# Kernel tuning notes

Measured on AMD Instinct MI355X. Metric: run time of the kernel, lower is better.

The kernel has to match this reference:

```python
import jax, jax.numpy as jnp
import numpy as np

N_USER, N_SPOT, D = 100000, 50000, 128
E_VISIT, E_REV, E_NEAR = 500000, 500000, 200000
P_DROP = 0.1


def _glorot(k, fan_in, fan_out):
    lim = jnp.sqrt(6.0 / (fan_in + fan_out))
    return jax.random.uniform(k, (fan_in, fan_out), jnp.float32, -lim, lim)


def setup_inputs() -> dict:
    key = jax.random.key(0)
    ks = jax.random.split(key, 14)
    return {
        "x_user": jax.random.normal(ks[0], (N_USER, D), jnp.float32),
        "x_spot": jax.random.normal(ks[1], (N_SPOT, D), jnp.float32),
        "W_visit_src": _glorot(ks[2], D, D),   # user side of (user,visit,spot)
        "W_visit_tgt": _glorot(ks[3], D, D),   # spot side of (user,visit,spot)
        "W_rev_src": _glorot(ks[4], D, D),     # spot side of (spot,visited_by,user)
        "W_rev_tgt": _glorot(ks[5], D, D),     # user side of (spot,visited_by,user)
        "W_near_src": _glorot(ks[6], D, D),    # (spot,near,spot)
        "W_near_tgt": _glorot(ks[7], D, D),
        "visit_src": jax.random.randint(ks[8], (E_VISIT,), 0, N_USER, jnp.int64),
        "visit_dst": jax.random.randint(ks[9], (E_VISIT,), 0, N_SPOT, jnp.int64),
        "rev_src": jax.random.randint(ks[10], (E_REV,), 0, N_SPOT, jnp.int64),
        "rev_dst": jax.random.randint(ks[11], (E_REV,), 0, N_USER, jnp.int64),
        "near_src": jax.random.randint(ks[12], (E_NEAR,), 0, N_SPOT, jnp.int64),
        "near_dst": jax.random.randint(ks[13], (E_NEAR,), 0, N_SPOT, jnp.int64),
    }


def _scatter_mean(vals, idx, n_seg):
    # scatter(..., reduce='mean') into zeros: empty segments stay 0
    s = jax.ops.segment_sum(vals, idx, num_segments=n_seg)
    c = jax.ops.segment_sum(jnp.ones((vals.shape[0],), vals.dtype), idx, num_segments=n_seg)
    return s / jnp.maximum(c, 1.0)[:, None]


def _edge_type(x_src, x_tgt, W_src, W_tgt, src_idx, dst_idx, n_tgt, dkey):
    src_p = x_src @ W_src                      # [N_src, D]
    tgt_p = x_tgt @ W_tgt                      # [N_tgt, D]
    g = src_p[src_idx]                         # gather per edge [E, D]
    keep = jax.random.bernoulli(dkey, 1.0 - P_DROP, g.shape)
    g = jnp.where(keep, g / (1.0 - P_DROP), jnp.zeros_like(g))  # dropout (training)
    return tgt_p + _scatter_mean(g, dst_idx, n_tgt)


def reference(x_user, x_spot, W_visit_src, W_visit_tgt, W_rev_src, W_rev_tgt,
              W_near_src, W_near_tgt, visit_src, visit_dst, rev_src, rev_dst,
              near_src, near_dst):
    dk = jax.random.key(1)
    spot_a = _edge_type(x_user, x_spot, W_visit_src, W_visit_tgt,
                        visit_src, visit_dst, N_SPOT, jax.random.fold_in(dk, 0))
    user_a = _edge_type(x_spot, x_user, W_rev_src, W_rev_tgt,
                        rev_src, rev_dst, N_USER, jax.random.fold_in(dk, 1))
    spot_b = _edge_type(x_spot, x_spot, W_near_src, W_near_tgt,
                        near_src, near_dst, N_SPOT, jax.random.fold_in(dk, 2))
    # div: spot receives from 2 edge types, user from 1
    out_user = jax.nn.relu(user_a / 1.0)
    out_spot = jax.nn.relu((spot_a + spot_b) / 2.0)
    # ReLU=True applies a second relu (no-op after the first, kept for faithfulness)
    return jax.nn.relu(out_user), jax.nn.relu(out_spot)
```

## Files before the change

kernel.cpp:

```cpp
#include <hip/hip_runtime.h>
#include <stdint.h>

#define DF 128
typedef unsigned short ushort_t;
typedef __attribute__((ext_vector_type(8))) short short8v;
typedef __attribute__((ext_vector_type(4))) float f32x4;

__host__ __device__ __forceinline__ unsigned rotl32(unsigned v, int r) {
  return __builtin_rotateleft32(v, (unsigned)r);
}

__host__ __device__ __forceinline__ void threefry2x32(
    unsigned k0, unsigned k1, unsigned c0, unsigned c1,
    unsigned& o0, unsigned& o1) {
  unsigned kx = k0 ^ k1 ^ 0x1BD11BDAu;
  unsigned x0 = c0 + k0;
  unsigned x1 = c1 + k1;
#define TF_R(r) { x0 += x1; x1 = rotl32(x1, r); x1 ^= x0; }
  TF_R(13) TF_R(15) TF_R(26) TF_R(6)
  x0 += k1; x1 += kx + 1u;
  TF_R(17) TF_R(29) TF_R(16) TF_R(24)
  x0 += kx; x1 += k0 + 2u;
  TF_R(13) TF_R(15) TF_R(26) TF_R(6)
  x0 += k0; x1 += k1 + 3u;
  TF_R(17) TF_R(29) TF_R(16) TF_R(24)
  x0 += k1; x1 += kx + 4u;
  TF_R(13) TF_R(15) TF_R(26) TF_R(6)
  x0 += kx; x1 += k0 + 5u;
#undef TF_R
  o0 = x0; o1 = x1;
}

#define KEEP_THR 0xE6666600u

__device__ __forceinline__ ushort_t f2bf(float f) {
  unsigned u = __float_as_uint(f);
  unsigned r = (u + 0x7fffu + ((u >> 16) & 1u)) >> 16;
  return (ushort_t)r;
}
__device__ __forceinline__ float bf2f(ushort_t h) {
  return __uint_as_float(((unsigned)h) << 16);
}
__device__ __forceinline__ unsigned umin_u(unsigned a, unsigned b) {
  return a < b ? a : b;
}

template <int EPI>
__global__ __launch_bounds__(256) void gemm_mfma(
    const float* __restrict__ X, const float* __restrict__ W1,
    const float* __restrict__ W2, int M,
    ushort_t* __restrict__ outB, float* __restrict__ outF,
    const ushort_t* __restrict__ m1, const ushort_t* __restrict__ m2) {
  __shared__ ushort_t Wt[DF][136];
  const int t = threadIdx.x;
  const int lane = t & 63;
  const int w = t >> 6;
  const int lr = lane & 15;
  const int kg = lane >> 4;
  const int rbase = blockIdx.x * 128;

#pragma unroll
  for (int i = 0; i < 16; ++i) {
    int q = t + i * 256;
    int k = q >> 5;
    int c4 = (q & 31) * 4;
    float4 wv = *reinterpret_cast<const float4*>(&W1[k * DF + c4]);
    if constexpr (EPI == 2) {
      float4 w2 = *reinterpret_cast<const float4*>(&W2[k * DF + c4]);
      wv.x += w2.x; wv.y += w2.y; wv.z += w2.z; wv.w += w2.w;
    }
    Wt[c4 + 0][k] = f2bf(wv.x);
    Wt[c4 + 1][k] = f2bf(wv.y);
    Wt[c4 + 2][k] = f2bf(wv.z);
    Wt[c4 + 3][k] = f2bf(wv.w);
  }
  __syncthreads();

  f32x4 acc[2][8];
#pragma unroll
  for (int rg = 0; rg < 2; ++rg)
#pragma unroll
    for (int n = 0; n < 8; ++n) acc[rg][n] = (f32x4){0.f, 0.f, 0.f, 0.f};

#pragma unroll
  for (int kt = 0; kt < 4; ++kt) {
    const int kb = kt * 32 + kg * 8;
    short8v a[2];
#pragma unroll
    for (int rg = 0; rg < 2; ++rg) {
      int r = rbase + w * 32 + rg * 16 + lr;
      float4 x0 = make_float4(0.f, 0.f, 0.f, 0.f);
      float4 x1 = x0;
      if (r < M) {
        x0 = *reinterpret_cast<const float4*>(&X[(size_t)r * DF + kb]);
        x1 = *reinterpret_cast<const float4*>(&X[(size_t)r * DF + kb + 4]);
      }
      short8v av;
      av[0] = (short)f2bf(x0.x); av[1] = (short)f2bf(x0.y);
      av[2] = (short)f2bf(x0.z); av[3] = (short)f2bf(x0.w);
      av[4] = (short)f2bf(x1.x); av[5] = (short)f2bf(x1.y);
      av[6] = (short)f2bf(x1.z); av[7] = (short)f2bf(x1.w);
      a[rg] = av;
    }
#pragma unroll
    for (int n = 0; n < 8; ++n) {
      short8v b = *reinterpret_cast<const short8v*>(&Wt[n * 16 + lr][kb]);
#pragma unroll
      for (int rg = 0; rg < 2; ++rg)
        acc[rg][n] = __builtin_amdgcn_mfma_f32_16x16x32_bf16(a[rg], b, acc[rg][n], 0, 0, 0);
    }
  }

#pragma unroll
  for (int rg = 0; rg < 2; ++rg) {
    const int rb = rbase + w * 32 + rg * 16 + kg * 4;
#pragma unroll
    for (int n = 0; n < 8; ++n) {
      const int col = n * 16 + lr;
#pragma unroll
      for (int j = 0; j < 4; ++j) {
        const int r = rb + j;
        if (r < M) {
          float vv = acc[rg][n][j];
          if (EPI == 0) {
            outB[(size_t)r * DF + col] = f2bf(vv);
          } else if (EPI == 1) {
            outF[(size_t)r * DF + col] =
                fmaxf(vv + bf2f(m1[(size_t)r * DF + col]), 0.f);
          } else {
            outF[(size_t)r * DF + col] =
                fmaxf(0.5f * (vv + bf2f(m1[(size_t)r * DF + col])
                                 + bf2f(m2[(size_t)r * DF + col])), 0.f);
          }
        }
      }
    }
  }
}

__global__ __launch_bounds__(256) void hist3(
    const int* __restrict__ vd, const int* __restrict__ rd,
    const int* __restrict__ nd, unsigned* __restrict__ deg_all,
    int Ev, int Er, int En, int segU, int segN) {
  int i = blockIdx.x * 256 + threadIdx.x;
  if (i < Ev) atomicAdd(&deg_all[vd[i]], 1u);
  else if (i < Ev + Er) atomicAdd(&deg_all[segU + rd[i - Ev]], 1u);
  else if (i < Ev + Er + En) atomicAdd(&deg_all[segN + nd[i - Ev - Er]], 1u);
}

#define SCAN_E 2048

__global__ __launch_bounds__(256) void scanA(
    const unsigned* __restrict__ deg, unsigned* __restrict__ bsum, int NT) {
  __shared__ unsigned sm[256];
  const int t = threadIdx.x;
  const int base = blockIdx.x * SCAN_E + t * 8;
  unsigned s = 0;
#pragma unroll
  for (int j = 0; j < 8; ++j) {
    int i = base + j;
    s += (i < NT) ? deg[i] : 0u;
  }
  sm[t] = s;
  __syncthreads();
  for (int off = 128; off; off >>= 1) {
    if (t < off) sm[t] += sm[t + off];
    __syncthreads();
  }
  if (t == 0) bsum[blockIdx.x] = sm[0];
}

__global__ __launch_bounds__(1024) void scanB(
    unsigned* __restrict__ bsum, unsigned* __restrict__ rp_all,
    int nb, int NT) {
  __shared__ unsigned sm[1024];
  const int t = threadIdx.x;
  unsigned v = (t < nb) ? bsum[t] : 0u;
  sm[t] = v;
  __syncthreads();
  for (int off = 1; off < 1024; off <<= 1) {
    unsigned u = (t >= off) ? sm[t - off] : 0u;
    __syncthreads();
    sm[t] += u;
    __syncthreads();
  }
  if (t < nb) bsum[t] = sm[t] - v;
  if (t == nb - 1) rp_all[NT] = sm[t];
}

__global__ __launch_bounds__(256) void scanC(
    const unsigned* __restrict__ deg, const unsigned* __restrict__ bsum,
    unsigned* __restrict__ rp, unsigned* __restrict__ cur, int NT) {
  __shared__ unsigned sm[256];
  const int t = threadIdx.x;
  const int base = blockIdx.x * SCAN_E + t * 8;
  unsigned vals[8];
  unsigned s = 0;
#pragma unroll
  for (int j = 0; j < 8; ++j) {
    int i = base + j;
    vals[j] = (i < NT) ? deg[i] : 0u;
    s += vals[j];
  }
  sm[t] = s;
  __syncthreads();
  for (int off = 1; off < 256; off <<= 1) {
    unsigned u = (t >= off) ? sm[t - off] : 0u;
    __syncthreads();
    sm[t] += u;
    __syncthreads();
  }
  unsigned run = bsum[blockIdx.x] + sm[t] - s;
#pragma unroll
  for (int j = 0; j < 8; ++j) {
    int i = base + j;
    if (i < NT) { rp[i] = run; cur[i] = run; }
    run += vals[j];
  }
}

__global__ __launch_bounds__(256) void fill3(
    const int* __restrict__ vs, const int* __restrict__ vd,
    const int* __restrict__ rs, const int* __restrict__ rd,
    const int* __restrict__ ns, const int* __restrict__ nd,
    unsigned* __restrict__ cur_all, uint2* __restrict__ es_all,
    int Ev, int Er, int En, int segU, int segN) {
  int i = blockIdx.x * 256 + threadIdx.x;
  if (i < Ev) {
    unsigned slot = atomicAdd(&cur_all[vd[i]], 1u);
    es_all[slot] = make_uint2((unsigned)i, (unsigned)vs[i]);
  } else if (i < Ev + Er) {
    int e = i - Ev;
    unsigned slot = atomicAdd(&cur_all[segU + rd[e]], 1u);
    es_all[slot] = make_uint2((unsigned)e, (unsigned)rs[e]);
  } else if (i < Ev + Er + En) {
    int e = i - Ev - Er;
    unsigned slot = atomicAdd(&cur_all[segN + nd[e]], 1u);
    es_all[slot] = make_uint2((unsigned)e, (unsigned)ns[e]);
  }
}

__global__ __launch_bounds__(256) void gather_reduce_all(
    const ushort_t* __restrict__ proj_v, const ushort_t* __restrict__ proj_r,
    const ushort_t* __restrict__ proj_n, const uint2* __restrict__ es,
    const unsigned* __restrict__ rp, ushort_t* __restrict__ accum_all,
    int NT, int segU, int segN, unsigned emax,
    unsigned kv0, unsigned kv1, unsigned kr0, unsigned kr1,
    unsigned kn0, unsigned kn1) {
  const int lane = threadIdx.x & 63;
  int d = blockIdx.x * 4 + (threadIdx.x >> 6);
  d = __builtin_amdgcn_readfirstlane(d);
  if (d >= NT) return;

  const ushort_t* proj;
  unsigned k0, k1;
  if (d < segU)      { proj = proj_v; k0 = kv0; k1 = kv1; }
  else if (d < segN) { proj = proj_r; k0 = kr0; k1 = kr1; }
  else               { proj = proj_n; k0 = kn0; k1 = kn1; }

  const unsigned b0 = __builtin_amdgcn_readfirstlane(rp[d]);
  const unsigned n  = __builtin_amdgcn_readfirstlane(rp[d + 1]) - b0;

  const bool hi = lane >= 32;
  const unsigned l31 = (unsigned)(lane & 31);
  const unsigned voff8 = l31 * 8u;

  const unsigned npairs = n >> 1;
  const unsigned odd = n & 1u;

  uint2 P0 = es[umin_u(b0, emax)];
  uint2 P1 = es[umin_u(b0 + 1u, emax)];
  unsigned eA = __builtin_amdgcn_readfirstlane(P0.x);
  unsigned sA = __builtin_amdgcn_readfirstlane(P0.y);
  unsigned eB = __builtin_amdgcn_readfirstlane(P1.x);
  unsigned sB = __builtin_amdgcn_readfirstlane(P1.y);

  float a0 = 0.f, a1 = 0.f, a2 = 0.f, a3 = 0.f;

  for (unsigned p = 0; p < npairs; ++p) {
    const unsigned src = hi ? sB : sA;
    const unsigned eid = hi ? eB : eA;
    const uint2 g = *reinterpret_cast<const uint2*>(
        reinterpret_cast<const char*>(proj) + ((size_t)src << 8) + voff8);
    uint2 Pn0 = es[umin_u(b0 + 2u * p + 2u, emax)];
    uint2 Pn1 = es[umin_u(b0 + 2u * p + 3u, emax)];

    const unsigned cb = eid * 128u + l31 * 4u;
    unsigned r0a, r0b, r1a, r1b, r2a, r2b, r3a, r3b;
    threefry2x32(k0, k1, 0u, cb + 0u, r0a, r0b);
    threefry2x32(k0, k1, 0u, cb + 1u, r1a, r1b);
    threefry2x32(k0, k1, 0u, cb + 2u, r2a, r2b);
    threefry2x32(k0, k1, 0u, cb + 3u, r3a, r3b);
    const float m0 = ((r0a ^ r0b) < KEEP_THR) ? (1.0f / 0.9f) : 0.f;
    const float m1 = ((r1a ^ r1b) < KEEP_THR) ? (1.0f / 0.9f) : 0.f;
    const float m2 = ((r2a ^ r2b) < KEEP_THR) ? (1.0f / 0.9f) : 0.f;
    const float m3 = ((r3a ^ r3b) < KEEP_THR) ? (1.0f / 0.9f) : 0.f;
    a0 = fmaf(__uint_as_float(g.x << 16), m0, a0);
    a1 = fmaf(__uint_as_float(g.x & 0xffff0000u), m1, a1);
    a2 = fmaf(__uint_as_float(g.y << 16), m2, a2);
    a3 = fmaf(__uint_as_float(g.y & 0xffff0000u), m3, a3);

    eA = __builtin_amdgcn_readfirstlane(Pn0.x);
    sA = __builtin_amdgcn_readfirstlane(Pn0.y);
    eB = __builtin_amdgcn_readfirstlane(Pn1.x);
    sB = __builtin_amdgcn_readfirstlane(Pn1.y);
  }

  if (odd) {
    const uint2 g = *reinterpret_cast<const uint2*>(
        reinterpret_cast<const char*>(proj) + ((size_t)sA << 8) + voff8);
    const unsigned cb = eA * 128u + l31 * 4u;
    unsigned r0a, r0b, r1a, r1b, r2a, r2b, r3a, r3b;
    threefry2x32(k0, k1, 0u, cb + 0u, r0a, r0b);
    threefry2x32(k0, k1, 0u, cb + 1u, r1a, r1b);
    threefry2x32(k0, k1, 0u, cb + 2u, r2a, r2b);
    threefry2x32(k0, k1, 0u, cb + 3u, r3a, r3b);
    const float sc = hi ? 0.f : (1.0f / 0.9f);
    const float m0 = ((r0a ^ r0b) < KEEP_THR) ? sc : 0.f;
    const float m1 = ((r1a ^ r1b) < KEEP_THR) ? sc : 0.f;
    const float m2 = ((r2a ^ r2b) < KEEP_THR) ? sc : 0.f;
    const float m3 = ((r3a ^ r3b) < KEEP_THR) ? sc : 0.f;
    a0 = fmaf(__uint_as_float(g.x << 16), m0, a0);
    a1 = fmaf(__uint_as_float(g.x & 0xffff0000u), m1, a1);
    a2 = fmaf(__uint_as_float(g.y << 16), m2, a2);
    a3 = fmaf(__uint_as_float(g.y & 0xffff0000u), m3, a3);
  }

  a0 += __shfl_xor(a0, 32);
  a1 += __shfl_xor(a1, 32);
  a2 += __shfl_xor(a2, 32);
  a3 += __shfl_xor(a3, 32);

  const float inv = 1.0f / fmaxf((float)n, 1.0f);
  const float u0 = hi ? a2 : a0;
  const float u1 = hi ? a3 : a1;
  const unsigned pk =
      ((unsigned)f2bf(u0 * inv)) | (((unsigned)f2bf(u1 * inv)) << 16);
  unsigned* out = reinterpret_cast<unsigned*>(accum_all) + (size_t)d * 64;
  out[2u * l31 + (hi ? 1u : 0u)] = pk;
}

extern "C" void kernel_launch(void* const* d_in, const int* in_sizes, int n_in,
                              void* d_out, int out_size, void* d_ws, size_t ws_size,
                              hipStream_t stream) {
  const float* x_user      = (const float*)d_in[0];
  const float* x_spot      = (const float*)d_in[1];
  const float* W_visit_src = (const float*)d_in[2];
  const float* W_visit_tgt = (const float*)d_in[3];
  const float* W_rev_src   = (const float*)d_in[4];
  const float* W_rev_tgt   = (const float*)d_in[5];
  const float* W_near_src  = (const float*)d_in[6];
  const float* W_near_tgt  = (const float*)d_in[7];
  const int* visit_src = (const int*)d_in[8];
  const int* visit_dst = (const int*)d_in[9];
  const int* rev_src   = (const int*)d_in[10];
  const int* rev_dst   = (const int*)d_in[11];
  const int* near_src  = (const int*)d_in[12];
  const int* near_dst  = (const int*)d_in[13];

  const int n_user = in_sizes[0] / DF;
  const int n_spot = in_sizes[1] / DF;
  const int e_visit = in_sizes[8];
  const int e_rev   = in_sizes[10];
  const int e_near  = in_sizes[12];

  float* out_user = (float*)d_out;
  float* out_spot = out_user + (size_t)n_user * DF;

  const int NT = n_spot + n_user + n_spot;
  const int segU = n_spot;
  const int segN = n_spot + n_user;
  const int etot = e_visit + e_rev + e_near;
  const unsigned emax = (unsigned)(etot - 1);

  char* ws = (char*)d_ws;
  size_t off = 0;
  auto alloc = [&](size_t bytes) -> void* {
    void* p = ws + off;
    off += (bytes + 255) & ~(size_t)255;
    return p;
  };
  ushort_t* proj_vs   = (ushort_t*)alloc((size_t)n_user * DF * 2);
  ushort_t* proj_rs   = (ushort_t*)alloc((size_t)n_spot * DF * 2);
  ushort_t* proj_ns   = (ushort_t*)alloc((size_t)n_spot * DF * 2);
  ushort_t* accum_all = (ushort_t*)alloc((size_t)NT * DF * 2);
  uint2*    es_all    = (uint2*)   alloc((size_t)etot * 8);
  unsigned* rp_all    = (unsigned*)alloc(((size_t)NT + 1) * 4);
  unsigned* cur_all   = (unsigned*)alloc((size_t)NT * 4);
  unsigned* deg_all   = (unsigned*)alloc((size_t)NT * 4);
  unsigned* bsum      = (unsigned*)alloc(4096);

  ushort_t* mean_sv = accum_all;
  ushort_t* mean_u  = accum_all + (size_t)segU * DF;
  ushort_t* mean_sn = accum_all + (size_t)segN * DF;

  unsigned kv0, kv1, kr0, kr1, kn0, kn1;
  threefry2x32(0u, 1u, 0u, 0u, kv0, kv1);
  threefry2x32(0u, 1u, 0u, 1u, kr0, kr1);
  threefry2x32(0u, 1u, 0u, 2u, kn0, kn1);

  dim3 blk(256);
  const int gb_user = (n_user + 127) / 128;
  const int gb_spot = (n_spot + 127) / 128;
  const int gb_e = (etot + 255) / 256;
  const int nb_scan = (NT + SCAN_E - 1) / SCAN_E;

  hipMemsetAsync(deg_all, 0, (size_t)NT * 4, stream);
  hist3<<<gb_e, blk, 0, stream>>>(visit_dst, rev_dst, near_dst, deg_all,
                                  e_visit, e_rev, e_near, segU, segN);
  scanA<<<nb_scan, blk, 0, stream>>>(deg_all, bsum, NT);
  scanB<<<1, 1024, 0, stream>>>(bsum, rp_all, nb_scan, NT);
  scanC<<<nb_scan, blk, 0, stream>>>(deg_all, bsum, rp_all, cur_all, NT);
  fill3<<<gb_e, blk, 0, stream>>>(visit_src, visit_dst, rev_src, rev_dst,
                                  near_src, near_dst, cur_all, es_all,
                                  e_visit, e_rev, e_near, segU, segN);

  gemm_mfma<0><<<gb_user, blk, 0, stream>>>(x_user, W_visit_src, nullptr, n_user,
                                            proj_vs, nullptr, nullptr, nullptr);
  gemm_mfma<0><<<gb_spot, blk, 0, stream>>>(x_spot, W_rev_src, nullptr, n_spot,
                                            proj_rs, nullptr, nullptr, nullptr);
  gemm_mfma<0><<<gb_spot, blk, 0, stream>>>(x_spot, W_near_src, nullptr, n_spot,
                                            proj_ns, nullptr, nullptr, nullptr);

  gather_reduce_all<<<(NT + 3) / 4, blk, 0, stream>>>(
      proj_vs, proj_rs, proj_ns, es_all, rp_all, accum_all,
      NT, segU, segN, emax, kv0, kv1, kr0, kr1, kn0, kn1);

  gemm_mfma<1><<<gb_user, blk, 0, stream>>>(x_user, W_rev_tgt, nullptr, n_user,
                                            nullptr, out_user, mean_u, nullptr);
  gemm_mfma<2><<<gb_spot, blk, 0, stream>>>(x_spot, W_visit_tgt, W_near_tgt, n_spot,
                                            nullptr, out_spot, mean_sv, mean_sn);
}
```

Baseline: 608.7 us.

## Merge GEMM launches and stage epilogue through LDS for coalesced stores

Combines the three source-projection GEMMs into one launch and the two target GEMMs into another, using block-index dispatch. The epilogue now stages accumulators in shared memory so global writes become 16-byte row-contiguous stores, and mean inputs are read as vectors. This replaces the scattered 2- and 4-byte stores of the MFMA layout and cuts launch overhead, at the cost of a larger shared-memory footprint and extra barriers.

```diff
diff --git a/kernel.cpp b/kernel.cpp
--- a/kernel.cpp
+++ b/kernel.cpp
@@ -38,26 +38,26 @@
   unsigned r = (u + 0x7fffu + ((u >> 16) & 1u)) >> 16;
   return (ushort_t)r;
 }
-__device__ __forceinline__ float bf2f(ushort_t h) {
-  return __uint_as_float(((unsigned)h) << 16);
+__device__ __forceinline__ float bf2f(unsigned h) {
+  return __uint_as_float(h << 16);
 }
 __device__ __forceinline__ unsigned umin_u(unsigned a, unsigned b) {
   return a < b ? a : b;
 }
 
-template <int EPI>
-__global__ __launch_bounds__(256) void gemm_mfma(
+#define WT(k, c) sm_u[(k) * 136 + (c)]
+#define CTB(r, c) sm_u[(r) * 144 + (c)]
+#define CTF(r, c) sm_f[(r) * 68 + (c)]
+
+__device__ __forceinline__ void gemm_core(
     const float* __restrict__ X, const float* __restrict__ W1,
-    const float* __restrict__ W2, int M,
-    ushort_t* __restrict__ outB, float* __restrict__ outF,
-    const ushort_t* __restrict__ m1, const ushort_t* __restrict__ m2) {
-  __shared__ ushort_t Wt[DF][136];
+    const float* __restrict__ W2, bool sumW, int M, int rbase,
+    ushort_t* sm_u, f32x4 acc[2][8]) {
   const int t = threadIdx.x;
   const int lane = t & 63;
   const int w = t >> 6;
   const int lr = lane & 15;
   const int kg = lane >> 4;
-  const int rbase = blockIdx.x * 128;
 
 #pragma unroll
   for (int i = 0; i < 16; ++i) {
@@ -65,18 +65,17 @@
     int k = q >> 5;
     int c4 = (q & 31) * 4;
     float4 wv = *reinterpret_cast<const float4*>(&W1[k * DF + c4]);
-    if constexpr (EPI == 2) {
+    if (sumW) {
       float4 w2 = *reinterpret_cast<const float4*>(&W2[k * DF + c4]);
       wv.x += w2.x; wv.y += w2.y; wv.z += w2.z; wv.w += w2.w;
     }
-    Wt[c4 + 0][k] = f2bf(wv.x);
-    Wt[c4 + 1][k] = f2bf(wv.y);
-    Wt[c4 + 2][k] = f2bf(wv.z);
-    Wt[c4 + 3][k] = f2bf(wv.w);
+    WT(c4 + 0, k) = f2bf(wv.x);
+    WT(c4 + 1, k) = f2bf(wv.y);
+    WT(c4 + 2, k) = f2bf(wv.z);
+    WT(c4 + 3, k) = f2bf(wv.w);
   }
   __syncthreads();
 
-  f32x4 acc[2][8];
 #pragma unroll
   for (int rg = 0; rg < 2; ++rg)
 #pragma unroll
@@ -104,38 +103,135 @@
     }
 #pragma unroll
     for (int n = 0; n < 8; ++n) {
-      short8v b = *reinterpret_cast<const short8v*>(&Wt[n * 16 + lr][kb]);
+      short8v b = *reinterpret_cast<const short8v*>(&WT(n * 16 + lr, kb));
 #pragma unroll
       for (int rg = 0; rg < 2; ++rg)
         acc[rg][n] = __builtin_amdgcn_mfma_f32_16x16x32_bf16(a[rg], b, acc[rg][n], 0, 0, 0);
     }
   }
-
+}
+
+__global__ __launch_bounds__(256) void proj3_gemm(
+    const float* __restrict__ x_user, const float* __restrict__ x_spot,
+    const float* __restrict__ Wv, const float* __restrict__ Wr,
+    const float* __restrict__ Wn, int n_user, int n_spot,
+    ushort_t* __restrict__ pv, ushort_t* __restrict__ pr,
+    ushort_t* __restrict__ pn, int gbU, int gbS) {
+  __shared__ __align__(16) ushort_t sm_u[18432];
+  const int b = blockIdx.x;
+  const float* X; const float* W; ushort_t* out; int M; int rbase;
+  if (b < gbU)            { X = x_user; W = Wv; out = pv; M = n_user; rbase = b * 128; }
+  else if (b < gbU + gbS) { X = x_spot; W = Wr; out = pr; M = n_spot; rbase = (b - gbU) * 128; }
+  else                    { X = x_spot; W = Wn; out = pn; M = n_spot; rbase = (b - gbU - gbS) * 128; }
+
+  f32x4 acc[2][8];
+  gemm_core(X, W, nullptr, false, M, rbase, sm_u, acc);
+
+  const int t = threadIdx.x;
+  const int lane = t & 63;
+  const int w = t >> 6;
+  const int lr = lane & 15;
+  const int kg = lane >> 4;
+
+  __syncthreads();
 #pragma unroll
   for (int rg = 0; rg < 2; ++rg) {
-    const int rb = rbase + w * 32 + rg * 16 + kg * 4;
+    const int rowb = w * 32 + rg * 16 + kg * 4;
 #pragma unroll
     for (int n = 0; n < 8; ++n) {
       const int col = n * 16 + lr;
 #pragma unroll
-      for (int j = 0; j < 4; ++j) {
-        const int r = rb + j;
-        if (r < M) {
-          float vv = acc[rg][n][j];
-          if (EPI == 0) {
-            outB[(size_t)r * DF + col] = f2bf(vv);
-          } else if (EPI == 1) {
-            outF[(size_t)r * DF + col] =
-                fmaxf(vv + bf2f(m1[(size_t)r * DF + col]), 0.f);
-          } else {
-            outF[(size_t)r * DF + col] =
-                fmaxf(0.5f * (vv + bf2f(m1[(size_t)r * DF + col])
-                                 + bf2f(m2[(size_t)r * DF + col])), 0.f);
-          }
-        }
+      for (int j = 0; j < 4; ++j) CTB(rowb + j, col) = f2bf(acc[rg][n][j]);
+    }
+  }
+  __syncthreads();
+#pragma unroll
+  for (int i = 0; i < 8; ++i) {
+    const int u = t + i * 256;
+    const int row = u >> 4, ch = u & 15;
+    const int grow = rbase + row;
+    if (grow < M)
+      *reinterpret_cast<uint4*>(&out[(size_t)grow * DF + ch * 8]) =
+          *reinterpret_cast<const uint4*>(&CTB(row, ch * 8));
+  }
+}
+
+__global__ __launch_bounds__(256) void final2_gemm(
+    const float* __restrict__ x_user, const float* __restrict__ x_spot,
+    const float* __restrict__ Wrt, const float* __restrict__ Wvt,
+    const float* __restrict__ Wnt, int n_user, int n_spot,
+    float* __restrict__ out_user, float* __restrict__ out_spot,
+    const ushort_t* __restrict__ mean_u, const ushort_t* __restrict__ mean_sv,
+    const ushort_t* __restrict__ mean_sn, int gbU) {
+  __shared__ __align__(16) ushort_t sm_u[17408];
+  float* sm_f_raw = reinterpret_cast<float*>(sm_u);
+#define sm_f sm_f_raw
+  const int b = blockIdx.x;
+  const bool epi2 = (b >= gbU);
+  const float* X; const float* W1; const float* W2; float* outF;
+  const ushort_t* m1; const ushort_t* m2; int M; int rbase;
+  if (!epi2) {
+    X = x_user; W1 = Wrt; W2 = nullptr; outF = out_user;
+    m1 = mean_u; m2 = nullptr; M = n_user; rbase = b * 128;
+  } else {
+    X = x_spot; W1 = Wvt; W2 = Wnt; outF = out_spot;
+    m1 = mean_sv; m2 = mean_sn; M = n_spot; rbase = (b - gbU) * 128;
+  }
+
+  f32x4 acc[2][8];
+  gemm_core(X, W1, W2, epi2, M, rbase, sm_u, acc);
+
+  const int t = threadIdx.x;
+  const int lane = t & 63;
+  const int w = t >> 6;
+  const int lr = lane & 15;
+  const int kg = lane >> 4;
+
+#pragma unroll
+  for (int h = 0; h < 2; ++h) {
+    __syncthreads();
+#pragma unroll
+    for (int rg = 0; rg < 2; ++rg) {
+      const int rowb = w * 32 + rg * 16 + kg * 4;
+#pragma unroll
+      for (int n2 = 0; n2 < 4; ++n2) {
+        const int n = h * 4 + n2;
+        const int col = n2 * 16 + lr;
+#pragma unroll
+        for (int j = 0; j < 4; ++j) CTF(rowb + j, col) = acc[rg][n][j];
       }
     }
-  }
+    __syncthreads();
+#pragma unroll
+    for (int i = 0; i < 8; ++i) {
+      const int u = t + i * 256;
+      const int row = u >> 4;
+      const int c4 = (u & 15) * 4;
+      const int grow = rbase + row;
+      if (grow < M) {
+        const float4 vv = *reinterpret_cast<const float4*>(&CTF(row, c4));
+        const int col = h * 64 + c4;
+        const uint2 mb = *reinterpret_cast<const uint2*>(&m1[(size_t)grow * DF + col]);
+        float a0 = bf2f(mb.x & 0xffffu), a1 = bf2f(mb.x >> 16);
+        float a2 = bf2f(mb.y & 0xffffu), a3 = bf2f(mb.y >> 16);
+        float4 r;
+        if (!epi2) {
+          r.x = fmaxf(vv.x + a0, 0.f);
+          r.y = fmaxf(vv.y + a1, 0.f);
+          r.z = fmaxf(vv.z + a2, 0.f);
+          r.w = fmaxf(vv.w + a3, 0.f);
+        } else {
+          const uint2 nb = *reinterpret_cast<const uint2*>(&m2[(size_t)grow * DF + col]);
+          r.x = fmaxf(0.5f * (vv.x + a0 + bf2f(nb.x & 0xffffu)), 0.f);
+          r.y = fmaxf(0.5f * (vv.y + a1 + bf2f(nb.x >> 16)), 0.f);
+          r.z = fmaxf(0.5f * (vv.z + a2 + bf2f(nb.y & 0xffffu)), 0.f);
+          r.w = fmaxf(0.5f * (vv.w + a3 + bf2f(nb.y >> 16)), 0.f);
+        }
+        *reinterpret_cast<float4*>(&outF[(size_t)grow * DF + col]) = r;
+      }
+    }
+  }
+#undef sm_f
 }
 
 __global__ __launch_bounds__(256) void hist3(
@@ -400,8 +496,8 @@
   threefry2x32(0u, 1u, 0u, 2u, kn0, kn1);
 
   dim3 blk(256);
-  const int gb_user = (n_user + 127) / 128;
-  const int gb_spot = (n_spot + 127) / 128;
+  const int gbU = (n_user + 127) / 128;
+  const int gbS = (n_spot + 127) / 128;
   const int gb_e = (etot + 255) / 256;
   const int nb_scan = (NT + SCAN_E - 1) / SCAN_E;
 
@@ -415,19 +511,15 @@
                                   near_src, near_dst, cur_all, es_all,
                                   e_visit, e_rev, e_near, segU, segN);
 
-  gemm_mfma<0><<<gb_user, blk, 0, stream>>>(x_user, W_visit_src, nullptr, n_user,
-                                            proj_vs, nullptr, nullptr, nullptr);
-  gemm_mfma<0><<<gb_spot, blk, 0, stream>>>(x_spot, W_rev_src, nullptr, n_spot,
-                                            proj_rs, nullptr, nullptr, nullptr);
-  gemm_mfma<0><<<gb_spot, blk, 0, stream>>>(x_spot, W_near_src, nullptr, n_spot,
-                                            proj_ns, nullptr, nullptr, nullptr);
+  proj3_gemm<<<gbU + 2 * gbS, blk, 0, stream>>>(
+      x_user, x_spot, W_visit_src, W_rev_src, W_near_src,
+      n_user, n_spot, proj_vs, proj_rs, proj_ns, gbU, gbS);
 
   gather_reduce_all<<<(NT + 3) / 4, blk, 0, stream>>>(
       proj_vs, proj_rs, proj_ns, es_all, rp_all, accum_all,
       NT, segU, segN, emax, kv0, kv1, kr0, kr1, kn0, kn1);
 
-  gemm_mfma<1><<<gb_user, blk, 0, stream>>>(x_user, W_rev_tgt, nullptr, n_user,
-                                            nullptr, out_user, mean_u, nullptr);
-  gemm_mfma<2><<<gb_spot, blk, 0, stream>>>(x_spot, W_visit_tgt, W_near_tgt, n_spot,
-                                            nullptr, out_spot, mean_sv, mean_sn);
-}
+  final2_gemm<<<gbU + gbS, blk, 0, stream>>>(
+      x_user, x_spot, W_rev_tgt, W_visit_tgt, W_near_tgt,
+      n_user, n_spot, out_user, out_spot, mean_u, mean_sv, mean_sn, gbU);
+}
```

Measured after the change: 559.9 us. -8.0%, faster.
